# Performance work log

Measured on AMD Instinct MI355X. Metric: run time of the kernel, lower is better.

The kernel has to match this reference:

```python
import jax, jax.numpy as jnp
import numpy as np

B = 2
D = 256; NH = 8; HD = D // NH; NL = 4; NP = 4; DFF = 1024
SHAPES = ((76, 106), (38, 53), (19, 27), (10, 14))  # (H, W) per level
LQ = sum(h * w for h, w in SHAPES)  # 10723
EPS = 1e-5


def _layer_norm(x, g, b):
    mu = jnp.mean(x, -1, keepdims=True)
    var = jnp.mean((x - mu) ** 2, -1, keepdims=True)
    return (x - mu) * jax.lax.rsqrt(var + EPS) * g + b


def _bilinear_sample(v_l, x, y, H, W):
    # v_l: (B, NH, H*W, HD); x, y: (B, NH, N) pixel coords (grid_sample align_corners=False, zero padding)
    x0 = jnp.floor(x); y0 = jnp.floor(y)
    fx = x - x0; fy = y - y0
    x0i = x0.astype(jnp.int32); y0i = y0.astype(jnp.int32)
    out = jnp.zeros(v_l.shape[:2] + (x.shape[-1], v_l.shape[-1]), v_l.dtype)
    for dx, wx in ((0, 1.0 - fx), (1, fx)):
        for dy, wy in ((0, 1.0 - fy), (1, fy)):
            xi = x0i + dx; yi = y0i + dy
            valid = (xi >= 0) & (xi < W) & (yi >= 0) & (yi < H)
            idx = jnp.clip(yi, 0, H - 1) * W + jnp.clip(xi, 0, W - 1)
            g = jnp.take_along_axis(v_l, idx[..., None], axis=2)  # (B,NH,N,HD)
            w = (wx * wy * valid.astype(v_l.dtype))[..., None]
            out = out + g * w
    return out


def _msdeform_attn(q, value, reference_points, shapes_np,
                   W_off, b_off, W_attn, b_attn, W_v, b_v, W_out, b_out):
    Bq, Lq, _ = q.shape
    v = (value @ W_v + b_v).reshape(Bq, -1, NH, HD).transpose(0, 2, 1, 3)  # (B,NH,Lv,HD)
    off = (q @ W_off + b_off).reshape(Bq, Lq, NH, NL, NP, 2)
    attn = jax.nn.softmax((q @ W_attn + b_attn).reshape(Bq, Lq, NH, NL * NP), -1)
    attn = attn.reshape(Bq, Lq, NH, NL, NP).transpose(0, 2, 1, 3, 4)  # (B,NH,Lq,NL,NP)
    # offset normalizer is (W, H) per level
    norm = jnp.asarray([[w, h] for h, w in shapes_np], q.dtype)  # (NL,2)
    loc = reference_points[:, :, None, :, None, :] + off / norm[None, None, None, :, None, :]
    loc = loc.transpose(0, 2, 1, 3, 4, 5)  # (B,NH,Lq,NL,NP,2), normalized [0,1] (x,y)
    out = jnp.zeros((Bq, NH, Lq, HD), q.dtype)
    start = 0
    for l in range(len(shapes_np)):
        H, W = int(shapes_np[l][0]), int(shapes_np[l][1])
        v_l = jax.lax.dynamic_slice_in_dim(v, start, H * W, axis=2)
        x = (loc[:, :, :, l, :, 0] * W - 0.5).reshape(Bq, NH, Lq * NP)
        y = (loc[:, :, :, l, :, 1] * H - 0.5).reshape(Bq, NH, Lq * NP)
        samp = _bilinear_sample(v_l, x, y, H, W).reshape(Bq, NH, Lq, NP, HD)
        out = out + jnp.einsum('bnqpd,bnqp->bnqd', samp, attn[:, :, :, l])
        start += H * W
    out = out.transpose(0, 2, 1, 3).reshape(Bq, Lq, D)
    return out @ W_out + b_out


def setup_inputs() -> dict:
    key = jax.random.key(0)
    ks = jax.random.split(key, 11)
    def init(k, shape, s=0.02):
        return (s * jax.random.normal(k, shape)).astype(jnp.float32)
    shapes = np.array(SHAPES, np.int32)
    lsi = np.concatenate([[0], np.cumsum(shapes[:, 0] * shapes[:, 1])[:-1]]).astype(np.int32)
    return {
        'query': jax.random.normal(ks[0], (B, LQ, D), jnp.float32),
        'query_pos': jax.random.normal(ks[1], (B, LQ, D), jnp.float32),
        'value': jax.random.normal(ks[2], (B, LQ, D), jnp.float32),
        'reference_points': jax.random.uniform(ks[3], (B, LQ, NL, 2), jnp.float32),
        'spatial_shapes': jnp.asarray(shapes),
        'level_start_index': jnp.asarray(lsi),
        'W_off': init(ks[4], (D, NH * NL * NP * 2)),
        'b_off': init(ks[5], (NH * NL * NP * 2,), 0.5),
        'W_attn': init(ks[6], (D, NH * NL * NP)),
        'b_attn': jnp.zeros((NH * NL * NP,), jnp.float32),
        'W_v': init(ks[7], (D, D)),
        'b_v': jnp.zeros((D,), jnp.float32),
        'W_out': init(ks[8], (D, D)),
        'b_out': jnp.zeros((D,), jnp.float32),
        'ln1_g': jnp.ones((D,), jnp.float32),
        'ln1_b': jnp.zeros((D,), jnp.float32),
        'W1': init(ks[9], (D, DFF)),
        'b1': jnp.zeros((DFF,), jnp.float32),
        'W2': init(ks[10], (DFF, D)),
        'b2': jnp.zeros((D,), jnp.float32),
        'ln2_g': jnp.ones((D,), jnp.float32),
        'ln2_b': jnp.zeros((D,), jnp.float32),
    }


def reference(query, query_pos, value, reference_points, spatial_shapes, level_start_index,
              W_off, b_off, W_attn, b_attn, W_v, b_v, W_out, b_out,
              ln1_g, ln1_b, W1, b1, W2, b2, ln2_g, ln2_b):
    shapes_np = np.asarray(spatial_shapes)  # static per-level (H, W)
    src2 = _msdeform_attn(query + query_pos, value, reference_points, shapes_np,
                          W_off, b_off, W_attn, b_attn, W_v, b_v, W_out, b_out)
    q = _layer_norm(query + src2, ln1_g, ln1_b)  # dropout is identity in eval mode
    ffn = jax.nn.relu(q @ W1 + b1) @ W2 + b2
    return _layer_norm(q + ffn, ln2_g, ln2_b)
```

## Files before the change

### kernel.cpp

```cpp
#include <hip/hip_runtime.h>
#include <math.h>

#define B_   2
#define LQ_  10723
#define D_   256
#define NH_  8
#define HD_  32
#define NL_  4
#define NP_  4
#define DFF_ 1024
#define M_   (B_ * LQ_)

typedef __attribute__((ext_vector_type(4))) float f32x4;
typedef __attribute__((ext_vector_type(8))) short short8;
typedef __attribute__((ext_vector_type(4))) unsigned short us4;
typedef __attribute__((ext_vector_type(8))) unsigned short us8;
typedef __attribute__((ext_vector_type(4))) unsigned int u32x4;

__device__ __forceinline__ unsigned short f2bf(float f) {
    union { float f; unsigned int u; } x; x.f = f;
    unsigned int r = x.u + 0x7FFF + ((x.u >> 16) & 1);
    return (unsigned short)(r >> 16);
}
__device__ __forceinline__ float bf2f(unsigned short u) {
    union { unsigned int u; float f; } x; x.u = (unsigned int)u << 16;
    return x.f;
}
__device__ __forceinline__ float bflo(unsigned int u) {
    union { unsigned int u; float f; } x; x.u = u << 16; return x.f;
}
__device__ __forceinline__ float bfhi(unsigned int u) {
    union { unsigned int u; float f; } x; x.u = u & 0xffff0000u; return x.f;
}

#define AS3U(p) ((__attribute__((address_space(3))) unsigned int*)(uintptr_t)(p))
#define AS1U(p) ((const __attribute__((address_space(1))) unsigned int*)(uintptr_t)(p))

__global__ __launch_bounds__(256) void prep_kernel(
    const float* __restrict__ Wv, const float* __restrict__ Woff,
    const float* __restrict__ Wattn, const float* __restrict__ Wout,
    const float* __restrict__ W1, const float* __restrict__ W2,
    const float* __restrict__ b_off, const float* __restrict__ b_attn,
    const float* __restrict__ value, const float* __restrict__ query,
    const float* __restrict__ qpos,
    unsigned short* __restrict__ WvT, unsigned short* __restrict__ WoaT,
    unsigned short* __restrict__ WoutT, unsigned short* __restrict__ W1T,
    unsigned short* __restrict__ W2T, float* __restrict__ b_oa,
    unsigned short* __restrict__ v16, unsigned short* __restrict__ q16, int n4)
{
    int idx = blockIdx.x * 256 + threadIdx.x;
    if (idx < 65536) {
        int n = idx >> 8, k = idx & 255;
        WvT[idx] = f2bf(Wv[k * 256 + n]);
    } else if (idx < 163840) {
        int l = idx - 65536; int n = l >> 8, k = l & 255;
        WoaT[l] = f2bf(n < 256 ? Woff[k * 256 + n] : Wattn[k * 128 + (n - 256)]);
    } else if (idx < 229376) {
        int l = idx - 163840; int n = l >> 8, k = l & 255;
        WoutT[l] = f2bf(Wout[k * 256 + n]);
    } else if (idx < 491520) {
        int l = idx - 229376; int n = l >> 8, k = l & 255;
        W1T[l] = f2bf(W1[k * 1024 + n]);
    } else if (idx < 753664) {
        int l = idx - 491520; int n = l >> 10, k = l & 1023;
        W2T[l] = f2bf(W2[k * 256 + n]);
    } else if (idx < 754048) {
        int l = idx - 753664;
        b_oa[l] = (l < 256) ? b_off[l] : b_attn[l - 256];
    } else if (idx < 754048 + n4) {
        int i = idx - 754048;
        float4 v = reinterpret_cast<const float4*>(value)[i];
        us4 r = { f2bf(v.x), f2bf(v.y), f2bf(v.z), f2bf(v.w) };
        reinterpret_cast<us4*>(v16)[i] = r;
    } else if (idx < 754048 + 2 * n4) {
        int j = idx - 754048 - n4;
        float4 va = reinterpret_cast<const float4*>(query)[j];
        float4 vb = reinterpret_cast<const float4*>(qpos)[j];
        us4 r = { f2bf(va.x + vb.x), f2bf(va.y + vb.y), f2bf(va.z + vb.z), f2bf(va.w + vb.w) };
        reinterpret_cast<us4*>(q16)[j] = r;
    }
}

__global__ __launch_bounds__(256) void gemm_pre(
    const unsigned short* __restrict__ v16, const unsigned short* __restrict__ q16,
    const unsigned short* __restrict__ WvT, const unsigned short* __restrict__ WoaT,
    const float* __restrict__ b_v, const float* __restrict__ b_oa,
    unsigned short* __restrict__ vph, float* __restrict__ oa)
{
    __shared__ unsigned short SM[2][2][128 * 32];

    const int i   = (int)blockIdx.y * 5 + (int)blockIdx.x;
    const int xcd = i & 7;
    const int jj  = i >> 3;
    const int by  = xcd * 21 + jj / 5;
    const int bx  = jj % 5;

    const bool is_v = (bx < 2);
    const unsigned short* A  = is_v ? v16 : q16;
    const unsigned short* BT = is_v ? WvT : WoaT;
    const float* bias = is_v ? b_v : b_oa;
    const int n0 = (is_v ? bx : bx - 2) * 128;
    const int K = 256;

    const int tid  = threadIdx.x;
    const int wave = tid >> 6;
    const int lane = tid & 63;
    const int m0 = by * 128;
    const int wr = (wave >> 1) * 64;
    const int wc = (wave & 1) * 64;

    f32x4 acc[4][4] = {};
    const int soff = wave * 1024 + lane * 16;

    auto stage = [&](int buf, int k0) {
        #pragma unroll
        for (int p = 0; p < 2; ++p) {
            const int off  = p * 4096 + soff;
            const int row  = off >> 6;
            const int colb = off & 63;
            int ar = m0 + row; ar = (ar < M_) ? ar : (M_ - 1);
            __builtin_amdgcn_global_load_lds(AS1U(A + (size_t)ar * K + k0 + (colb >> 1)),
                AS3U(&SM[0][buf][(p * 4096 + wave * 1024) >> 1]), 16, 0, 0);
            __builtin_amdgcn_global_load_lds(AS1U(BT + (size_t)(n0 + row) * K + k0 + (colb >> 1)),
                AS3U(&SM[1][buf][(p * 4096 + wave * 1024) >> 1]), 16, 0, 0);
        }
    };

    stage(0, 0);
    __syncthreads();
    int cur = 0;
    for (int t = 0; t < 8; ++t) {
        if (t + 1 < 8) stage(cur ^ 1, (t + 1) * 32);
        const int fr = lane & 15;
        const int kb = (lane >> 4) * 8;
        short8 af[4], bf[4];
        #pragma unroll
        for (int m = 0; m < 4; ++m)
            af[m] = *reinterpret_cast<const short8*>(&SM[0][cur][(wr + m * 16 + fr) * 32 + kb]);
        #pragma unroll
        for (int n = 0; n < 4; ++n)
            bf[n] = *reinterpret_cast<const short8*>(&SM[1][cur][(wc + n * 16 + fr) * 32 + kb]);
        #pragma unroll
        for (int m = 0; m < 4; ++m)
            #pragma unroll
            for (int n = 0; n < 4; ++n)
                acc[m][n] = __builtin_amdgcn_mfma_f32_16x16x32_bf16(af[m], bf[n], acc[m][n], 0, 0, 0);
        if (t + 1 < 8) { __syncthreads(); cur ^= 1; }
    }

    const int fr = lane & 15;
    const int r0 = (lane >> 4) * 4;
    if (is_v) {
        __syncthreads();
        unsigned short* Ct = &SM[0][0][0];
        #pragma unroll
        for (int n = 0; n < 4; ++n) {
            const float bv = bias[n0 + wc + n * 16 + fr];
            #pragma unroll
            for (int m = 0; m < 4; ++m)
                #pragma unroll
                for (int r = 0; r < 4; ++r)
                    Ct[(wr + m * 16 + r0 + r) * 128 + wc + n * 16 + fr] = f2bf(acc[m][n][r] + bv);
        }
        __syncthreads();
        #pragma unroll
        for (int pass = 0; pass < 8; ++pass) {
            const int r  = pass * 16 + (tid >> 4);
            const int c8 = (tid & 15) * 8;
            const int row = m0 + r;
            if (row < M_) {
                const int col = n0 + c8;
                const int bb = (row >= LQ_) ? 1 : 0;
                const int lvv = row - bb * LQ_;
                const int hh = col >> 5, dd = col & 31;
                us8 v = *reinterpret_cast<const us8*>(&Ct[r * 128 + c8]);
                *reinterpret_cast<us8*>(&vph[(((size_t)bb * NH_ + hh) * LQ_ + lvv) * 32 + dd]) = v;
            }
        }
    } else {
        #pragma unroll
        for (int n = 0; n < 4; ++n) {
            const int col = n0 + wc + n * 16 + fr;
            const float bv = bias[col];
            #pragma unroll
            for (int m = 0; m < 4; ++m) {
                #pragma unroll
                for (int r = 0; r < 4; ++r) {
                    const int row = m0 + wr + m * 16 + r0 + r;
                    if (row < M_) oa[(size_t)row * 384 + col] = acc[m][n][r] + bv;
                }
            }
        }
    }
}

__global__ __launch_bounds__(256) void gemm_ffn1(
    const unsigned short* __restrict__ A,
    const unsigned short* __restrict__ BT,
    const float* __restrict__ bias,
    unsigned short* __restrict__ Cout,
    int M, int N, int K)
{
    __shared__ unsigned short SM[2][2][128 * 32];

    const int i   = (int)blockIdx.y * 8 + (int)blockIdx.x;
    const int xcd = i & 7;
    const int jj  = i >> 3;
    const int by  = xcd * 21 + (jj >> 3);
    const int bx  = jj & 7;

    const int tid  = threadIdx.x;
    const int wave = tid >> 6;
    const int lane = tid & 63;
    const int m0 = by * 128;
    const int n0 = bx * 128;
    const int wr = (wave >> 1) * 64;
    const int wc = (wave & 1) * 64;

    f32x4 acc[4][4] = {};
    const int soff = wave * 1024 + lane * 16;

    auto stage = [&](int buf, int k0) {
        #pragma unroll
        for (int p = 0; p < 2; ++p) {
            const int off  = p * 4096 + soff;
            const int row  = off >> 6;
            const int colb = off & 63;
            int ar = m0 + row; ar = (ar < M) ? ar : (M - 1);
            __builtin_amdgcn_global_load_lds(AS1U(A + (size_t)ar * K + k0 + (colb >> 1)),
                AS3U(&SM[0][buf][(p * 4096 + wave * 1024) >> 1]), 16, 0, 0);
            __builtin_amdgcn_global_load_lds(AS1U(BT + (size_t)(n0 + row) * K + k0 + (colb >> 1)),
                AS3U(&SM[1][buf][(p * 4096 + wave * 1024) >> 1]), 16, 0, 0);
        }
    };

    const int nt = K >> 5;
    stage(0, 0);
    __syncthreads();
    int cur = 0;
    for (int t = 0; t < nt; ++t) {
        if (t + 1 < nt) stage(cur ^ 1, (t + 1) * 32);
        const int fr = lane & 15;
        const int kb = (lane >> 4) * 8;
        short8 af[4], bf[4];
        #pragma unroll
        for (int m = 0; m < 4; ++m)
            af[m] = *reinterpret_cast<const short8*>(&SM[0][cur][(wr + m * 16 + fr) * 32 + kb]);
        #pragma unroll
        for (int n = 0; n < 4; ++n)
            bf[n] = *reinterpret_cast<const short8*>(&SM[1][cur][(wc + n * 16 + fr) * 32 + kb]);
        #pragma unroll
        for (int m = 0; m < 4; ++m)
            #pragma unroll
            for (int n = 0; n < 4; ++n)
                acc[m][n] = __builtin_amdgcn_mfma_f32_16x16x32_bf16(af[m], bf[n], acc[m][n], 0, 0, 0);
        if (t + 1 < nt) { __syncthreads(); cur ^= 1; }
    }

    const int fr = lane & 15;
    const int r0 = (lane >> 4) * 4;
    __syncthreads();
    unsigned short* Ct = &SM[0][0][0];
    #pragma unroll
    for (int n = 0; n < 4; ++n) {
        const float bv = bias[n0 + wc + n * 16 + fr];
        #pragma unroll
        for (int m = 0; m < 4; ++m)
            #pragma unroll
            for (int r = 0; r < 4; ++r)
                Ct[(wr + m * 16 + r0 + r) * 128 + wc + n * 16 + fr] = f2bf(fmaxf(acc[m][n][r] + bv, 0.f));
    }
    __syncthreads();
    #pragma unroll
    for (int pass = 0; pass < 8; ++pass) {
        const int r  = pass * 16 + (tid >> 4);
        const int c8 = (tid & 15) * 8;
        const int row = m0 + r;
        if (row < M) {
            us8 v = *reinterpret_cast<const us8*>(&Ct[r * 128 + c8]);
            *reinterpret_cast<us8*>(&Cout[(size_t)row * N + n0 + c8]) = v;
        }
    }
}

template<int RES_BF16, int OUT_F32>
__global__ __launch_bounds__(512) void gemm_ln(
    const unsigned short* __restrict__ A,
    const unsigned short* __restrict__ BT,
    const float* __restrict__ bias,
    const void* __restrict__ resp,
    const float* __restrict__ g,
    const float* __restrict__ beta,
    void* __restrict__ outp,
    int M, int K)
{
    __shared__ unsigned short As[2][64 * 32];
    __shared__ unsigned short Bs[2][256 * 32];
    __shared__ float2 sRed[4][64];

    const int tid  = threadIdx.x;
    const int wave = tid >> 6;
    const int lane = tid & 63;
    const int m0 = blockIdx.x * 64;
    const int wr = (wave >> 2) * 32;
    const int wc = (wave & 3) * 64;

    f32x4 acc[2][4] = {};

    auto stage = [&](int buf, int k0) {
        if (tid < 256) {
            const int off  = tid * 16;
            const int row  = off >> 6;
            const int colb = off & 63;
            int ar = m0 + row; ar = (ar < M) ? ar : (M - 1);
            __builtin_amdgcn_global_load_lds(AS1U(A + (size_t)ar * K + k0 + (colb >> 1)),
                AS3U(&As[buf][(wave * 1024) >> 1]), 16, 0, 0);
        }
        #pragma unroll
        for (int p = 0; p < 2; ++p) {
            const int off  = p * 8192 + tid * 16;
            const int row  = off >> 6;
            const int colb = off & 63;
            __builtin_amdgcn_global_load_lds(AS1U(BT + (size_t)row * K + k0 + (colb >> 1)),
                AS3U(&Bs[buf][(p * 8192 + wave * 1024) >> 1]), 16, 0, 0);
        }
    };

    const int nt = K >> 5;
    stage(0, 0);
    __syncthreads();
    int cur = 0;
    for (int t = 0; t < nt; ++t) {
        if (t + 1 < nt) stage(cur ^ 1, (t + 1) * 32);
        const int fr = lane & 15;
        const int kb = (lane >> 4) * 8;
        short8 af[2], bf[4];
        #pragma unroll
        for (int m = 0; m < 2; ++m)
            af[m] = *reinterpret_cast<const short8*>(&As[cur][(wr + m * 16 + fr) * 32 + kb]);
        #pragma unroll
        for (int n = 0; n < 4; ++n)
            bf[n] = *reinterpret_cast<const short8*>(&Bs[cur][(wc + n * 16 + fr) * 32 + kb]);
        #pragma unroll
        for (int m = 0; m < 2; ++m)
            #pragma unroll
            for (int n = 0; n < 4; ++n)
                acc[m][n] = __builtin_amdgcn_mfma_f32_16x16x32_bf16(af[m], bf[n], acc[m][n], 0, 0, 0);
        if (t + 1 < nt) { __syncthreads(); cur ^= 1; }
    }

    const int fr = lane & 15;
    const int r0 = (lane >> 4) * 4;
    float biasv[4], gv[4], bev[4];
    #pragma unroll
    for (int n = 0; n < 4; ++n) {
        const int col = wc + n * 16 + fr;
        biasv[n] = bias[col]; gv[n] = g[col]; bev[n] = beta[col];
    }
    #pragma unroll
    for (int m = 0; m < 2; ++m) {
        #pragma unroll
        for (int r = 0; r < 4; ++r) {
            int row = m0 + wr + m * 16 + r0 + r;
            int rr = (row < M) ? row : (M - 1);
            if (RES_BF16) {
                const unsigned short* rp = (const unsigned short*)resp + (size_t)rr * 256;
                #pragma unroll
                for (int n = 0; n < 4; ++n)
                    acc[m][n][r] += biasv[n] + bf2f(rp[wc + n * 16 + fr]);
            } else {
                const float* rp = (const float*)resp + (size_t)rr * 256;
                #pragma unroll
                for (int n = 0; n < 4; ++n)
                    acc[m][n][r] += biasv[n] + rp[wc + n * 16 + fr];
            }
        }
    }
    #pragma unroll
    for (int m = 0; m < 2; ++m) {
        #pragma unroll
        for (int r = 0; r < 4; ++r) {
            float sx = 0.f, sxx = 0.f;
            #pragma unroll
            for (int n = 0; n < 4; ++n) { float t = acc[m][n][r]; sx += t; sxx += t * t; }
            #pragma unroll
            for (int mask = 1; mask < 16; mask <<= 1) {
                sx  += __shfl_xor(sx, mask);
                sxx += __shfl_xor(sxx, mask);
            }
            if (fr == 0) sRed[wave & 3][wr + m * 16 + r0 + r] = make_float2(sx, sxx);
        }
    }
    __syncthreads();
    unsigned short* Ct = &Bs[0][0];
    #pragma unroll
    for (int m = 0; m < 2; ++m) {
        #pragma unroll
        for (int r = 0; r < 4; ++r) {
            const int lr = wr + m * 16 + r0 + r;
            float2 a0 = sRed[0][lr], a1 = sRed[1][lr], a2 = sRed[2][lr], a3 = sRed[3][lr];
            const float S  = a0.x + a1.x + a2.x + a3.x;
            const float SS = a0.y + a1.y + a2.y + a3.y;
            const float mean = S * (1.f / 256.f);
            const float var  = SS * (1.f / 256.f) - mean * mean;
            const float rstd = rsqrtf(var + 1e-5f);
            const int row = m0 + lr;
            #pragma unroll
            for (int n = 0; n < 4; ++n) {
                const int col = wc + n * 16 + fr;
                const float y = (acc[m][n][r] - mean) * rstd * gv[n] + bev[n];
                if (OUT_F32) {
                    if (row < M) ((float*)outp)[(size_t)row * 256 + col] = y;
                } else {
                    Ct[lr * 256 + col] = f2bf(y);
                }
            }
        }
    }
    if (!OUT_F32) {
        __syncthreads();
        unsigned short* o16 = (unsigned short*)outp;
        #pragma unroll
        for (int pass = 0; pass < 4; ++pass) {
            const int rrow = pass * 16 + (tid >> 5);
            const int cb = (tid & 31) * 8;
            const int grow = m0 + rrow;
            if (grow < M) {
                us8 v = *reinterpret_cast<const us8*>(&Ct[rrow * 256 + cb]);
                *reinterpret_cast<us8*>(&o16[(size_t)grow * 256 + cb]) = v;
            }
        }
    }
}

__global__ __launch_bounds__(256) void msdeform_kernel(
    const unsigned short* __restrict__ vproj_h, const float* __restrict__ offattn,
    const float* __restrict__ refp, unsigned short* __restrict__ msout)
{
    __shared__ int4   sIdx[4][16][17];
    __shared__ float4 sWgt[4][16][17];

    const int bh = blockIdx.x & 15;
    const int qc = blockIdx.x >> 4;
    const int b  = bh >> 3;
    const int h  = bh & 7;
    const int wave = threadIdx.x >> 6;
    const int lane = threadIdx.x & 63;
    const int qq = lane >> 2;
    const int j  = lane & 3;
    const int lv = qc * 64 + wave * 16 + qq;
    if (lv >= LQ_) return;
    const int bq = b * LQ_ + lv;

    const float4 oA = *reinterpret_cast<const float4*>(offattn + (size_t)bq * 384 + h * 32 + 8 * j);
    const float4 oB = *reinterpret_cast<const float4*>(offattn + (size_t)bq * 384 + h * 32 + 8 * j + 4);
    const float4 lg = *reinterpret_cast<const float4*>(offattn + (size_t)bq * 384 + 256 + h * 16 + 4 * j);
    const float2 rp = *reinterpret_cast<const float2*>(refp + (size_t)bq * 8 + 2 * j);

    const float Wf[4] = {106.f, 53.f, 27.f, 14.f};
    const float Hf[4] = {76.f, 38.f, 19.f, 10.f};
    const int   Wi[4] = {106, 53, 27, 14};
    const int   Hi[4] = {76, 38, 19, 10};
    const int   St[4] = {0, 8056, 10070, 10583};

    float mx = fmaxf(fmaxf(lg.x, lg.y), fmaxf(lg.z, lg.w));
    mx = fmaxf(mx, __shfl_xor(mx, 1));
    mx = fmaxf(mx, __shfl_xor(mx, 2));
    const float e0 = __expf(lg.x - mx), e1 = __expf(lg.y - mx);
    const float e2 = __expf(lg.z - mx), e3 = __expf(lg.w - mx);
    float s = e0 + e1 + e2 + e3;
    s += __shfl_xor(s, 1); s += __shfl_xor(s, 2);
    const float inv = 1.f / s;

    const int W = Wi[j], H = Hi[j];
    const float Wff = Wf[j], Hff = Hf[j];
    const int base = St[j];
    const float oxs[4] = {oA.x, oA.z, oB.x, oB.z};
    const float oys[4] = {oA.y, oA.w, oB.y, oB.w};
    const float ews[4] = {e0, e1, e2, e3};

    #pragma unroll
    for (int i = 0; i < 4; ++i) {
        const float aw = ews[i] * inv;
        const float x = fmaf(rp.x, Wff, oxs[i]) - 0.5f;
        const float y = fmaf(rp.y, Hff, oys[i]) - 0.5f;
        const float xf = floorf(x), yf = floorf(y);
        const float fx = x - xf, fy = y - yf;
        const int x0 = (int)xf, y0 = (int)yf;
        const float gx = 1.f - fx, gy = 1.f - fy;
        const bool vx0 = (x0 >= 0) && (x0 < W);
        const bool vx1 = (x0 + 1 >= 0) && (x0 + 1 < W);
        const bool vy0 = (y0 >= 0) && (y0 < H);
        const bool vy1 = (y0 + 1 >= 0) && (y0 + 1 < H);
        const int xc0 = min(max(x0, 0), W - 1);
        const int xc1 = min(max(x0 + 1, 0), W - 1);
        const int yr0 = min(max(y0, 0), H - 1) * W;
        const int yr1 = min(max(y0 + 1, 0), H - 1) * W;
        int4 iv; float4 wv;
        iv.x = (base + yr0 + xc0) << 6;  wv.x = (vx0 && vy0) ? gx * gy * aw : 0.f;
        iv.y = (base + yr0 + xc1) << 6;  wv.y = (vx1 && vy0) ? fx * gy * aw : 0.f;
        iv.z = (base + yr1 + xc0) << 6;  wv.z = (vx0 && vy1) ? gx * fy * aw : 0.f;
        iv.w = (base + yr1 + xc1) << 6;  wv.w = (vx1 && vy1) ? fx * fy * aw : 0.f;
        sIdx[wave][qq][4 * j + i] = iv;
        sWgt[wave][qq][4 * j + i] = wv;
    }

    const char* vb = (const char*)(vproj_h + (size_t)bh * LQ_ * 32) + j * 16;
    f32x4 accA = {0.f, 0.f, 0.f, 0.f};
    f32x4 accB = {0.f, 0.f, 0.f, 0.f};

    int4 iv0 = sIdx[wave][qq][0];
    u32x4 a0 = *reinterpret_cast<const u32x4*>(vb + (unsigned)iv0.x);
    u32x4 a1 = *reinterpret_cast<const u32x4*>(vb + (unsigned)iv0.y);
    u32x4 a2 = *reinterpret_cast<const u32x4*>(vb + (unsigned)iv0.z);
    u32x4 a3 = *reinterpret_cast<const u32x4*>(vb + (unsigned)iv0.w);

    #pragma unroll
    for (int p = 0; p < 16; ++p) {
        u32x4 b0, b1, b2, b3;
        if (p < 15) {
            const int4 nv = sIdx[wave][qq][p + 1];
            b0 = *reinterpret_cast<const u32x4*>(vb + (unsigned)nv.x);
            b1 = *reinterpret_cast<const u32x4*>(vb + (unsigned)nv.y);
            b2 = *reinterpret_cast<const u32x4*>(vb + (unsigned)nv.z);
            b3 = *reinterpret_cast<const u32x4*>(vb + (unsigned)nv.w);
        }
        const float4 wv = sWgt[wave][qq][p];
        accA[0] = fmaf(wv.x, bflo(a0.x), accA[0]); accA[1] = fmaf(wv.x, bfhi(a0.x), accA[1]);
        accA[2] = fmaf(wv.x, bflo(a0.y), accA[2]); accA[3] = fmaf(wv.x, bfhi(a0.y), accA[3]);
        accB[0] = fmaf(wv.x, bflo(a0.z), accB[0]); accB[1] = fmaf(wv.x, bfhi(a0.z), accB[1]);
        accB[2] = fmaf(wv.x, bflo(a0.w), accB[2]); accB[3] = fmaf(wv.x, bfhi(a0.w), accB[3]);
        accA[0] = fmaf(wv.y, bflo(a1.x), accA[0]); accA[1] = fmaf(wv.y, bfhi(a1.x), accA[1]);
        accA[2] = fmaf(wv.y, bflo(a1.y), accA[2]); accA[3] = fmaf(wv.y, bfhi(a1.y), accA[3]);
        accB[0] = fmaf(wv.y, bflo(a1.z), accB[0]); accB[1] = fmaf(wv.y, bfhi(a1.z), accB[1]);
        accB[2] = fmaf(wv.y, bflo(a1.w), accB[2]); accB[3] = fmaf(wv.y, bfhi(a1.w), accB[3]);
        accA[0] = fmaf(wv.z, bflo(a2.x), accA[0]); accA[1] = fmaf(wv.z, bfhi(a2.x), accA[1]);
        accA[2] = fmaf(wv.z, bflo(a2.y), accA[2]); accA[3] = fmaf(wv.z, bfhi(a2.y), accA[3]);
        accB[0] = fmaf(wv.z, bflo(a2.z), accB[0]); accB[1] = fmaf(wv.z, bfhi(a2.z), accB[1]);
        accB[2] = fmaf(wv.z, bflo(a2.w), accB[2]); accB[3] = fmaf(wv.z, bfhi(a2.w), accB[3]);
        accA[0] = fmaf(wv.w, bflo(a3.x), accA[0]); accA[1] = fmaf(wv.w, bfhi(a3.x), accA[1]);
        accA[2] = fmaf(wv.w, bflo(a3.y), accA[2]); accA[3] = fmaf(wv.w, bfhi(a3.y), accA[3]);
        accB[0] = fmaf(wv.w, bflo(a3.z), accB[0]); accB[1] = fmaf(wv.w, bfhi(a3.z), accB[1]);
        accB[2] = fmaf(wv.w, bflo(a3.w), accB[2]); accB[3] = fmaf(wv.w, bfhi(a3.w), accB[3]);
        a0 = b0; a1 = b1; a2 = b2; a3 = b3;
    }
    us8 r = { f2bf(accA[0]), f2bf(accA[1]), f2bf(accA[2]), f2bf(accA[3]),
              f2bf(accB[0]), f2bf(accB[1]), f2bf(accB[2]), f2bf(accB[3]) };
    *reinterpret_cast<us8*>(msout + (size_t)bq * 256 + h * 32 + j * 8) = r;
}

extern "C" void kernel_launch(void* const* d_in, const int* in_sizes, int n_in,
                              void* d_out, int out_size, void* d_ws, size_t ws_size,
                              hipStream_t stream) {
    const float* query = (const float*)d_in[0];
    const float* qpos  = (const float*)d_in[1];
    const float* value = (const float*)d_in[2];
    const float* refp  = (const float*)d_in[3];
    const float* W_off  = (const float*)d_in[6];
    const float* b_off  = (const float*)d_in[7];
    const float* W_attn = (const float*)d_in[8];
    const float* b_attn = (const float*)d_in[9];
    const float* W_v    = (const float*)d_in[10];
    const float* b_v    = (const float*)d_in[11];
    const float* W_out  = (const float*)d_in[12];
    const float* b_out  = (const float*)d_in[13];
    const float* ln1_g  = (const float*)d_in[14];
    const float* ln1_b  = (const float*)d_in[15];
    const float* W1     = (const float*)d_in[16];
    const float* b1     = (const float*)d_in[17];
    const float* W2     = (const float*)d_in[18];
    const float* b2     = (const float*)d_in[19];
    const float* ln2_g  = (const float*)d_in[20];
    const float* ln2_b  = (const float*)d_in[21];
    float* out = (float*)d_out;

    unsigned short* WvT   = (unsigned short*)d_ws;
    unsigned short* WoaT  = WvT   + 65536;
    unsigned short* WoutT = WoaT  + 98304;
    unsigned short* W1T   = WoutT + 65536;
    unsigned short* W2T   = W1T   + 262144;
    float* b_oa = (float*)(W2T + 262144);
    uint8_t* base = (uint8_t*)(b_oa + 384);
    base = (uint8_t*)(((uintptr_t)base + 255) & ~(uintptr_t)255);

    const size_t A = (size_t)M_ * D_;
    unsigned short* R_v16  = (unsigned short*)base;
    unsigned short* R_q16  = R_v16 + A;
    unsigned short* R_vph  = R_q16 + A;
    float* R_oa  = (float*)(R_vph + A);
    unsigned short* R_h16 = (unsigned short*)(R_oa + (size_t)M_ * 384);

    const dim3 blk(256);
    auto cdiv = [](size_t a, size_t b) { return (unsigned)((a + b - 1) / b); };

    const int n4 = (int)(A / 4);
    prep_kernel<<<cdiv(754048 + 2 * (size_t)n4, 256), blk, 0, stream>>>(
        W_v, W_off, W_attn, W_out, W1, W2, b_off, b_attn, value, query, qpos,
        WvT, WoaT, WoutT, W1T, W2T, b_oa, R_v16, R_q16, n4);

    const unsigned MT = (M_ + 127) / 128;
    gemm_pre<<<dim3(5, MT), blk, 0, stream>>>(
        R_v16, R_q16, WvT, WoaT, b_v, b_oa, R_vph, R_oa);
    const unsigned nQC = cdiv(LQ_, 64);
    msdeform_kernel<<<dim3(nQC * 16), blk, 0, stream>>>(R_vph, R_oa, refp, R_q16);
    gemm_ln<0, 0><<<dim3(cdiv(M_, 64)), dim3(512), 0, stream>>>(
        R_q16, WoutT, b_out, query, ln1_g, ln1_b, R_v16, M_, 256);
    gemm_ffn1<<<dim3(8, MT), blk, 0, stream>>>(R_v16, W1T, b1, R_h16, M_, 1024, 256);
    gemm_ln<1, 1><<<dim3(cdiv(M_, 64)), dim3(512), 0, stream>>>(
        R_h16, W2T, b2, R_v16, ln2_g, ln2_b, out, M_, 1024);
}
```

Measured before the change: 143.1 us.

## Fuse FFN up-projection, ReLU, down-projection and LayerNorm into one kernel

Replaces the separate FFN1 GEMM (writing a bf16 hidden tensor of M x 1024) and the FFN2+LayerNorm GEMM with a single kernel. Each 64-row block keeps its input tile in LDS, computes the hidden activations in 128-column chunks, applies bias and ReLU, and accumulates the down-projection directly. This removes the global round trip of the hidden tensor and one launch. In exchange, every block re-streams all of W1 and W2 with little double buffering and many barriers, and the grid has only about 336 blocks of 512 threads, which may hurt occupancy and MFMA utilisation.

```diff
diff --git a/kernel.cpp b/kernel.cpp
--- a/kernel.cpp
+++ b/kernel.cpp
@@ -194,104 +194,14 @@
     }
 }
 
-__global__ __launch_bounds__(256) void gemm_ffn1(
+__global__ __launch_bounds__(512) void gemm_ln1(
     const unsigned short* __restrict__ A,
     const unsigned short* __restrict__ BT,
     const float* __restrict__ bias,
-    unsigned short* __restrict__ Cout,
-    int M, int N, int K)
-{
-    __shared__ unsigned short SM[2][2][128 * 32];
-
-    const int i   = (int)blockIdx.y * 8 + (int)blockIdx.x;
-    const int xcd = i & 7;
-    const int jj  = i >> 3;
-    const int by  = xcd * 21 + (jj >> 3);
-    const int bx  = jj & 7;
-
-    const int tid  = threadIdx.x;
-    const int wave = tid >> 6;
-    const int lane = tid & 63;
-    const int m0 = by * 128;
-    const int n0 = bx * 128;
-    const int wr = (wave >> 1) * 64;
-    const int wc = (wave & 1) * 64;
-
-    f32x4 acc[4][4] = {};
-    const int soff = wave * 1024 + lane * 16;
-
-    auto stage = [&](int buf, int k0) {
-        #pragma unroll
-        for (int p = 0; p < 2; ++p) {
-            const int off  = p * 4096 + soff;
-            const int row  = off >> 6;
-            const int colb = off & 63;
-            int ar = m0 + row; ar = (ar < M) ? ar : (M - 1);
-            __builtin_amdgcn_global_load_lds(AS1U(A + (size_t)ar * K + k0 + (colb >> 1)),
-                AS3U(&SM[0][buf][(p * 4096 + wave * 1024) >> 1]), 16, 0, 0);
-            __builtin_amdgcn_global_load_lds(AS1U(BT + (size_t)(n0 + row) * K + k0 + (colb >> 1)),
-                AS3U(&SM[1][buf][(p * 4096 + wave * 1024) >> 1]), 16, 0, 0);
-        }
-    };
-
-    const int nt = K >> 5;
-    stage(0, 0);
-    __syncthreads();
-    int cur = 0;
-    for (int t = 0; t < nt; ++t) {
-        if (t + 1 < nt) stage(cur ^ 1, (t + 1) * 32);
-        const int fr = lane & 15;
-        const int kb = (lane >> 4) * 8;
-        short8 af[4], bf[4];
-        #pragma unroll
-        for (int m = 0; m < 4; ++m)
-            af[m] = *reinterpret_cast<const short8*>(&SM[0][cur][(wr + m * 16 + fr) * 32 + kb]);
-        #pragma unroll
-        for (int n = 0; n < 4; ++n)
-            bf[n] = *reinterpret_cast<const short8*>(&SM[1][cur][(wc + n * 16 + fr) * 32 + kb]);
-        #pragma unroll
-        for (int m = 0; m < 4; ++m)
-            #pragma unroll
-            for (int n = 0; n < 4; ++n)
-                acc[m][n] = __builtin_amdgcn_mfma_f32_16x16x32_bf16(af[m], bf[n], acc[m][n], 0, 0, 0);
-        if (t + 1 < nt) { __syncthreads(); cur ^= 1; }
-    }
-
-    const int fr = lane & 15;
-    const int r0 = (lane >> 4) * 4;
-    __syncthreads();
-    unsigned short* Ct = &SM[0][0][0];
-    #pragma unroll
-    for (int n = 0; n < 4; ++n) {
-        const float bv = bias[n0 + wc + n * 16 + fr];
-        #pragma unroll
-        for (int m = 0; m < 4; ++m)
-            #pragma unroll
-            for (int r = 0; r < 4; ++r)
-                Ct[(wr + m * 16 + r0 + r) * 128 + wc + n * 16 + fr] = f2bf(fmaxf(acc[m][n][r] + bv, 0.f));
-    }
-    __syncthreads();
-    #pragma unroll
-    for (int pass = 0; pass < 8; ++pass) {
-        const int r  = pass * 16 + (tid >> 4);
-        const int c8 = (tid & 15) * 8;
-        const int row = m0 + r;
-        if (row < M) {
-            us8 v = *reinterpret_cast<const us8*>(&Ct[r * 128 + c8]);
-            *reinterpret_cast<us8*>(&Cout[(size_t)row * N + n0 + c8]) = v;
-        }
-    }
-}
-
-template<int RES_BF16, int OUT_F32>
-__global__ __launch_bounds__(512) void gemm_ln(
-    const unsigned short* __restrict__ A,
-    const unsigned short* __restrict__ BT,
-    const float* __restrict__ bias,
-    const void* __restrict__ resp,
+    const float* __restrict__ res,
     const float* __restrict__ g,
     const float* __restrict__ beta,
-    void* __restrict__ outp,
+    unsigned short* __restrict__ out16,
     int M, int K)
 {
     __shared__ unsigned short As[2][64 * 32];
@@ -363,17 +273,10 @@
         for (int r = 0; r < 4; ++r) {
             int row = m0 + wr + m * 16 + r0 + r;
             int rr = (row < M) ? row : (M - 1);
-            if (RES_BF16) {
-                const unsigned short* rp = (const unsigned short*)resp + (size_t)rr * 256;
-                #pragma unroll
-                for (int n = 0; n < 4; ++n)
-                    acc[m][n][r] += biasv[n] + bf2f(rp[wc + n * 16 + fr]);
-            } else {
-                const float* rp = (const float*)resp + (size_t)rr * 256;
-                #pragma unroll
-                for (int n = 0; n < 4; ++n)
-                    acc[m][n][r] += biasv[n] + rp[wc + n * 16 + fr];
-            }
+            const float* rp = res + (size_t)rr * 256;
+            #pragma unroll
+            for (int n = 0; n < 4; ++n)
+                acc[m][n][r] += biasv[n] + rp[wc + n * 16 + fr];
         }
     }
     #pragma unroll
@@ -404,30 +307,190 @@
             const float mean = S * (1.f / 256.f);
             const float var  = SS * (1.f / 256.f) - mean * mean;
             const float rstd = rsqrtf(var + 1e-5f);
-            const int row = m0 + lr;
             #pragma unroll
             for (int n = 0; n < 4; ++n) {
                 const int col = wc + n * 16 + fr;
                 const float y = (acc[m][n][r] - mean) * rstd * gv[n] + bev[n];
-                if (OUT_F32) {
-                    if (row < M) ((float*)outp)[(size_t)row * 256 + col] = y;
-                } else {
-                    Ct[lr * 256 + col] = f2bf(y);
+                Ct[lr * 256 + col] = f2bf(y);
+            }
+        }
+    }
+    __syncthreads();
+    #pragma unroll
+    for (int pass = 0; pass < 4; ++pass) {
+        const int rrow = pass * 16 + (tid >> 5);
+        const int cb = (tid & 31) * 8;
+        const int grow = m0 + rrow;
+        if (grow < M) {
+            us8 v = *reinterpret_cast<const us8*>(&Ct[rrow * 256 + cb]);
+            *reinterpret_cast<us8*>(&out16[(size_t)grow * 256 + cb]) = v;
+        }
+    }
+}
+
+#define AQ_S 264
+#define HC_S 136
+__global__ __launch_bounds__(512) void gemm_ffn_ln(
+    const unsigned short* __restrict__ Aq16,
+    const unsigned short* __restrict__ W1T,
+    const float* __restrict__ b1,
+    const unsigned short* __restrict__ W2T,
+    const float* __restrict__ b2,
+    const float* __restrict__ g,
+    const float* __restrict__ beta,
+    float* __restrict__ outf,
+    int M)
+{
+    __shared__ unsigned short Aq[64 * AQ_S];
+    __shared__ unsigned short Hc[64 * HC_S];
+    __shared__ unsigned short Wst[2][128 * 32];
+    __shared__ float2 sRed[4][64];
+
+    const int tid  = threadIdx.x;
+    const int wave = tid >> 6;
+    const int lane = tid & 63;
+    const int m0 = blockIdx.x * 64;
+    const int fr = lane & 15;
+    const int kb = (lane >> 4) * 8;
+    const int r0 = (lane >> 4) * 4;
+
+    #pragma unroll
+    for (int p = 0; p < 4; ++p) {
+        const int off = p * 8192 + tid * 16;
+        const int row = off >> 9;
+        const int colb = off & 511;
+        int ar = m0 + row; ar = (ar < M) ? ar : (M - 1);
+        us8 v = *reinterpret_cast<const us8*>(Aq16 + (size_t)ar * 256 + (colb >> 1));
+        *reinterpret_cast<us8*>(Aq + row * AQ_S + (colb >> 1)) = v;
+    }
+
+    const int wrA = (wave >> 2) * 32, wcA = (wave & 3) * 32;
+    const int wrB = (wave >> 2) * 32, wcB = (wave & 3) * 64;
+
+    f32x4 accC[2][4] = {};
+
+    __syncthreads();
+
+    for (int c = 0; c < 8; ++c) {
+        f32x4 accH[2][2] = {};
+        {
+            const int off = tid * 16;
+            const int row = off >> 6;
+            __builtin_amdgcn_global_load_lds(
+                AS1U(W1T + (size_t)(c * 128 + row) * 256 + ((off & 63) >> 1)),
+                AS3U(&Wst[0][off >> 1]), 16, 0, 0);
+        }
+        __syncthreads();
+        for (int t = 0; t < 8; ++t) {
+            if (t + 1 < 8) {
+                const int off = tid * 16;
+                const int row = off >> 6;
+                __builtin_amdgcn_global_load_lds(
+                    AS1U(W1T + (size_t)(c * 128 + row) * 256 + (t + 1) * 32 + ((off & 63) >> 1)),
+                    AS3U(&Wst[(t + 1) & 1][off >> 1]), 16, 0, 0);
+            }
+            short8 af[2], bf[2];
+            #pragma unroll
+            for (int m = 0; m < 2; ++m)
+                af[m] = *reinterpret_cast<const short8*>(Aq + (wrA + m * 16 + fr) * AQ_S + t * 32 + kb);
+            #pragma unroll
+            for (int n = 0; n < 2; ++n)
+                bf[n] = *reinterpret_cast<const short8*>(&Wst[t & 1][(wcA + n * 16 + fr) * 32 + kb]);
+            #pragma unroll
+            for (int m = 0; m < 2; ++m)
+                #pragma unroll
+                for (int n = 0; n < 2; ++n)
+                    accH[m][n] = __builtin_amdgcn_mfma_f32_16x16x32_bf16(af[m], bf[n], accH[m][n], 0, 0, 0);
+            if (t + 1 < 8) __syncthreads();
+        }
+        #pragma unroll
+        for (int n = 0; n < 2; ++n) {
+            const float bv = b1[c * 128 + wcA + n * 16 + fr];
+            #pragma unroll
+            for (int m = 0; m < 2; ++m)
+                #pragma unroll
+                for (int r = 0; r < 4; ++r)
+                    Hc[(wrA + m * 16 + r0 + r) * HC_S + wcA + n * 16 + fr] =
+                        f2bf(fmaxf(accH[m][r == 0 ? n : n][r] + bv, 0.f));
+        }
+        __syncthreads();
+
+        for (int tt = 0; tt < 4; ++tt) {
+            #pragma unroll
+            for (int p = 0; p < 2; ++p) {
+                const int off = p * 8192 + tid * 16;
+                const int row = off >> 6;
+                __builtin_amdgcn_global_load_lds(
+                    AS1U(W2T + (size_t)row * 1024 + c * 128 + tt * 32 + ((off & 63) >> 1)),
+                    AS3U(&Wst[0][0] + (off >> 1)), 16, 0, 0);
+            }
+            __syncthreads();
+            short8 af[2], bf[4];
+            #pragma unroll
+            for (int m = 0; m < 2; ++m)
+                af[m] = *reinterpret_cast<const short8*>(Hc + (wrB + m * 16 + fr) * HC_S + tt * 32 + kb);
+            #pragma unroll
+            for (int n = 0; n < 4; ++n)
+                bf[n] = *reinterpret_cast<const short8*>(&Wst[0][0] + (wcB + n * 16 + fr) * 32 + kb);
+            #pragma unroll
+            for (int m = 0; m < 2; ++m)
+                #pragma unroll
+                for (int n = 0; n < 4; ++n)
+                    accC[m][n] = __builtin_amdgcn_mfma_f32_16x16x32_bf16(af[m], bf[n], accC[m][n], 0, 0, 0);
+            __syncthreads();
+        }
+    }
+
+    float b2v[4], gv[4], bev[4];
+    #pragma unroll
+    for (int n = 0; n < 4; ++n) {
+        const int col = wcB + n * 16 + fr;
+        b2v[n] = b2[col]; gv[n] = g[col]; bev[n] = beta[col];
+    }
+    #pragma unroll
+    for (int m = 0; m < 2; ++m) {
+        #pragma unroll
+        for (int r = 0; r < 4; ++r) {
+            const int lr = wrB + m * 16 + r0 + r;
+            #pragma unroll
+            for (int n = 0; n < 4; ++n)
+                accC[m][n][r] += b2v[n] + bf2f(Aq[lr * AQ_S + wcB + n * 16 + fr]);
+        }
+    }
+    #pragma unroll
+    for (int m = 0; m < 2; ++m) {
+        #pragma unroll
+        for (int r = 0; r < 4; ++r) {
+            float sx = 0.f, sxx = 0.f;
+            #pragma unroll
+            for (int n = 0; n < 4; ++n) { float t = accC[m][n][r]; sx += t; sxx += t * t; }
+            #pragma unroll
+            for (int mask = 1; mask < 16; mask <<= 1) {
+                sx  += __shfl_xor(sx, mask);
+                sxx += __shfl_xor(sxx, mask);
+            }
+            if (fr == 0) sRed[wave & 3][wrB + m * 16 + r0 + r] = make_float2(sx, sxx);
+        }
+    }
+    __syncthreads();
+    #pragma unroll
+    for (int m = 0; m < 2; ++m) {
+        #pragma unroll
+        for (int r = 0; r < 4; ++r) {
+            const int lr = wrB + m * 16 + r0 + r;
+            float2 a0 = sRed[0][lr], a1 = sRed[1][lr], a2 = sRed[2][lr], a3 = sRed[3][lr];
+            const float S  = a0.x + a1.x + a2.x + a3.x;
+            const float SS = a0.y + a1.y + a2.y + a3.y;
+            const float mean = S * (1.f / 256.f);
+            const float var  = SS * (1.f / 256.f) - mean * mean;
+            const float rstd = rsqrtf(var + 1e-5f);
+            const int row = m0 + lr;
+            if (row < M) {
+                #pragma unroll
+                for (int n = 0; n < 4; ++n) {
+                    const int col = wcB + n * 16 + fr;
+                    outf[(size_t)row * 256 + col] = (accC[m][n][r] - mean) * rstd * gv[n] + bev[n];
                 }
-            }
-        }
-    }
-    if (!OUT_F32) {
-        __syncthreads();
-        unsigned short* o16 = (unsigned short*)outp;
-        #pragma unroll
-        for (int pass = 0; pass < 4; ++pass) {
-            const int rrow = pass * 16 + (tid >> 5);
-            const int cb = (tid & 31) * 8;
-            const int grow = m0 + rrow;
-            if (grow < M) {
-                us8 v = *reinterpret_cast<const us8*>(&Ct[rrow * 256 + cb]);
-                *reinterpret_cast<us8*>(&o16[(size_t)grow * 256 + cb]) = v;
             }
         }
     }
@@ -588,7 +651,6 @@
     unsigned short* R_q16  = R_v16 + A;
     unsigned short* R_vph  = R_q16 + A;
     float* R_oa  = (float*)(R_vph + A);
-    unsigned short* R_h16 = (unsigned short*)(R_oa + (size_t)M_ * 384);
 
     const dim3 blk(256);
     auto cdiv = [](size_t a, size_t b) { return (unsigned)((a + b - 1) / b); };
@@ -603,9 +665,8 @@
         R_v16, R_q16, WvT, WoaT, b_v, b_oa, R_vph, R_oa);
     const unsigned nQC = cdiv(LQ_, 64);
     msdeform_kernel<<<dim3(nQC * 16), blk, 0, stream>>>(R_vph, R_oa, refp, R_q16);
-    gemm_ln<0, 0><<<dim3(cdiv(M_, 64)), dim3(512), 0, stream>>>(
+    gemm_ln1<<<dim3(cdiv(M_, 64)), dim3(512), 0, stream>>>(
         R_q16, WoutT, b_out, query, ln1_g, ln1_b, R_v16, M_, 256);
-    gemm_ffn1<<<dim3(8, MT), blk, 0, stream>>>(R_v16, W1T, b1, R_h16, M_, 1024, 256);
-    gemm_ln<1, 1><<<dim3(cdiv(M_, 64)), dim3(512), 0, stream>>>(
-        R_h16, W2T, b2, R_v16, ln2_g, ln2_b, out, M_, 1024);
-}
+    gemm_ffn_ln<<<dim3(cdiv(M_, 64)), dim3(512), 0, stream>>>(
+        R_v16, W1T, b1, W2T, b2, ln2_g, ln2_b, out, M_);
+}
```

After: 148.0 us. +3.4%, slower.
